# Kernel tuning notes

Hardware: AMD Instinct MI355X
Metric: run time of the kernel (lower is better)

## Reference

```python
import jax, jax.numpy as jnp
import numpy as np

B, H = 8192, 768


def _mk_linear(key, fan_in, fan_out):
    k1, k2 = jax.random.split(key)
    lim = 1.0 / np.sqrt(fan_in)
    W = jax.random.uniform(k1, (fan_out, fan_in), jnp.float32, -lim, lim)
    b = jax.random.uniform(k2, (fan_out,), jnp.float32, -lim, lim)
    return W, b


def setup_inputs() -> dict:
    key = jax.random.key(0)
    ks = jax.random.split(key, 6)
    modal_a = jax.random.normal(ks[0], (B, H), jnp.float32)
    modal_b = jax.random.normal(ks[1], (B, H), jnp.float32)
    W1m, b1m = _mk_linear(ks[2], H, H)
    W2m, b2m = _mk_linear(ks[3], H, H)
    W1v, b1v = _mk_linear(ks[4], H, H)
    W2v, b2v = _mk_linear(ks[5], H, H)
    return {"modal_a": modal_a, "modal_b": modal_b,
            "W1m": W1m, "b1m": b1m, "W2m": W2m, "b2m": b2m,
            "W1v": W1v, "b1v": b1v, "W2v": W2v, "b2v": b2v}


def reference(modal_a, modal_b, W1m, b1m, W2m, b2m, W1v, b1v, W2v, b2v):
    # mlp_mu: Linear -> Tanh -> Linear
    mu = jnp.tanh(modal_a @ W1m.T + b1m) @ W2m.T + b2m              # [B,H]
    # mlp_logvar: Linear -> Tanh -> Linear -> Tanh
    logvar = jnp.tanh(jnp.tanh(modal_a @ W1v.T + b1v) @ W2v.T + b2v)  # [B,H]
    inv_var = jnp.exp(-logvar)

    positive = -(mu - modal_b) ** 2 * 0.5 * inv_var                  # [B,H]

    # mean_j (mu[j] - mu[i])^2 = E[mu^2] - 2*mu[i]*E[mu] + mu[i]^2  (per feature dim)
    # Algebraic reduction of the O(B^2*H) tile in the original code.
    mu_mean = jnp.mean(mu, axis=0)                                   # [H]
    mu_sq_mean = jnp.mean(mu * mu, axis=0)                           # [H]
    pair_sq = mu_sq_mean - 2.0 * mu * mu_mean + mu * mu              # [B,H]
    negative = -pair_sq * 0.5 * inv_var                              # [B,H]

    pos_sum = jnp.sum(positive, axis=-1)                             # [B]
    neg_sum = jnp.sum(negative, axis=-1)                             # [B]
    lld = jnp.mean(pos_sum)
    bound = jnp.mean(pos_sum - neg_sum)
    return (lld, bound)
```

## Files before the change

### kernel.cpp

```cpp
#include <hip/hip_runtime.h>
#include <math.h>

typedef float v4f __attribute__((ext_vector_type(4)));
typedef short bf16x8 __attribute__((ext_vector_type(8)));

#define AS1 __attribute__((address_space(1)))
#define AS3 __attribute__((address_space(3)))

static constexpr int Bn = 8192;
static constexpr int Hn = 768;
static constexpr float invB = 1.0f / 8192.0f;

__device__ __forceinline__ short f32_to_bf16(float x) {
    union { float f; unsigned u; } v; v.f = x;
    unsigned r = (v.u + 0x7FFFu + ((v.u >> 16) & 1u)) >> 16;
    return (short)r;
}

__device__ __forceinline__ float fast_tanh(float x) {
    float xc = fminf(fmaxf(x, -15.0f), 15.0f);
    float e = __expf(2.0f * xc);
    float r = __builtin_amdgcn_rcpf(e + 1.0f);
    return 1.0f - 2.0f * r;
}

__global__ void prep_kernel(const float* __restrict__ A,
                            const float* __restrict__ W1m, const float* __restrict__ W2m,
                            const float* __restrict__ W1v, const float* __restrict__ W2v,
                            short* __restrict__ A_bf,
                            short* __restrict__ W1m_bf, short* __restrict__ W2m_bf,
                            short* __restrict__ W1v_bf, short* __restrict__ W2v_bf,
                            float* __restrict__ zbuf, int nzero) {
    const int tid = blockIdx.x * blockDim.x + threadIdx.x;
    if (tid < nzero) zbuf[tid] = 0.0f;
    constexpr int A4 = Bn * Hn / 4;
    constexpr int W4 = Hn * Hn / 4;
    const int total = A4 + 4 * W4;
    const int stride = gridDim.x * blockDim.x;
    for (int i = tid; i < total; i += stride) {
        const float* s; short* d; int j;
        if (i < A4) { s = A; d = A_bf; j = i; }
        else {
            int k = i - A4; int w = k / W4; j = k - w * W4;
            s = (w == 0) ? W1m : (w == 1) ? W2m : (w == 2) ? W1v : W2v;
            d = (w == 0) ? W1m_bf : (w == 1) ? W2m_bf : (w == 2) ? W1v_bf : W2v_bf;
        }
        float4 v = ((const float4*)s)[j];
        short4 o;
        o.x = f32_to_bf16(v.x); o.y = f32_to_bf16(v.y);
        o.z = f32_to_bf16(v.z); o.w = f32_to_bf16(v.w);
        ((short4*)d)[j] = o;
    }
}

__launch_bounds__(256, 2)
__global__ void gemm_l1(const short* __restrict__ A_g,
                        const short* __restrict__ Wm_g, const short* __restrict__ Wv_g,
                        const float* __restrict__ bm, const float* __restrict__ bv,
                        short* __restrict__ outm, short* __restrict__ outv) {
    constexpr int K = Hn;
    __shared__ __align__(16) short smem[24576];
    short* As = smem;
    short* Wms = smem + 8192;
    short* Wvs = smem + 16384;

    const int t = threadIdx.x;
    const int row0 = blockIdx.x * 128;
    const int col0 = blockIdx.y * 128;
    const int w = t >> 6, lane = t & 63;
    const int wm = w >> 1, wn = w & 1;
    const int lr = lane & 15, quad = lane >> 4;

    const int rt = t >> 3;
    const int bsrc = (t & 7) ^ (rt & 7);

    const short* pA[4]; const short* pWm[4]; const short* pWv[4];
#pragma unroll
    for (int i = 0; i < 4; ++i) {
        pA[i]  = A_g  + (size_t)(row0 + i * 32 + rt) * K + bsrc * 8;
        pWm[i] = Wm_g + (size_t)(col0 + i * 32 + rt) * K + bsrc * 8;
        pWv[i] = Wv_g + (size_t)(col0 + i * 32 + rt) * K + bsrc * 8;
    }

    v4f accm[4][4] = {}, accv[4][4] = {};

    for (int k0 = 0; k0 < K; k0 += 64) {
#pragma unroll
        for (int i = 0; i < 4; ++i) {
            __builtin_amdgcn_global_load_lds((AS1 void*)pA[i],  (AS3 void*)&As[i * 2048 + t * 8], 16, 0, 0);
            __builtin_amdgcn_global_load_lds((AS1 void*)pWm[i], (AS3 void*)&Wms[i * 2048 + t * 8], 16, 0, 0);
            __builtin_amdgcn_global_load_lds((AS1 void*)pWv[i], (AS3 void*)&Wvs[i * 2048 + t * 8], 16, 0, 0);
            pA[i] += 64; pWm[i] += 64; pWv[i] += 64;
        }
        __syncthreads();
#pragma unroll
        for (int s = 0; s < 2; ++s) {
            const int kb = s * 4 + quad;
            bf16x8 af[4], fm[4], fv[4];
#pragma unroll
            for (int mt = 0; mt < 4; ++mt) {
                int m = wm * 64 + mt * 16 + lr;
                af[mt] = *(const bf16x8*)&As[m * 64 + ((kb ^ (m & 7)) << 3)];
            }
#pragma unroll
            for (int nt = 0; nt < 4; ++nt) {
                int n = wn * 64 + nt * 16 + lr;
                int off = n * 64 + ((kb ^ (n & 7)) << 3);
                fm[nt] = *(const bf16x8*)&Wms[off];
                fv[nt] = *(const bf16x8*)&Wvs[off];
            }
#pragma unroll
            for (int mt = 0; mt < 4; ++mt)
#pragma unroll
                for (int nt = 0; nt < 4; ++nt) {
                    accm[mt][nt] = __builtin_amdgcn_mfma_f32_16x16x32_bf16(af[mt], fm[nt], accm[mt][nt], 0, 0, 0);
                    accv[mt][nt] = __builtin_amdgcn_mfma_f32_16x16x32_bf16(af[mt], fv[nt], accv[mt][nt], 0, 0, 0);
                }
        }
        __syncthreads();
    }

#pragma unroll
    for (int br = 0; br < 2; ++br) {
        const float* bias = br ? bv : bm;
        short* out = br ? outv : outm;
#pragma unroll
        for (int nt = 0; nt < 4; ++nt) {
            const int col_l = wn * 64 + nt * 16 + lr;
            const float bc = bias[col0 + col_l];
#pragma unroll
            for (int mt = 0; mt < 4; ++mt) {
#pragma unroll
                for (int r = 0; r < 4; ++r) {
                    const int row_l = wm * 64 + mt * 16 + quad * 4 + r;
                    float v = (br ? accv[mt][nt][r] : accm[mt][nt][r]) + bc;
                    smem[row_l * 136 + col_l] = f32_to_bf16(fast_tanh(v));
                }
            }
        }
        __syncthreads();
#pragma unroll
        for (int p = 0; p < 8; ++p) {
            const int c = p * 256 + t;
            const int row = c >> 4, rem = c & 15;
            bf16x8 v = *(const bf16x8*)&smem[row * 136 + rem * 8];
            *(bf16x8*)&out[(size_t)(row0 + row) * Hn + col0 + rem * 8] = v;
        }
        __syncthreads();
    }
}

__launch_bounds__(256, 2)
__global__ void gemm_l2(const short* __restrict__ Am_g, const short* __restrict__ Av_g,
                        const short* __restrict__ Wm_g, const short* __restrict__ Wv_g,
                        const float* __restrict__ bm, const float* __restrict__ bv,
                        const float* __restrict__ mb,
                        float* __restrict__ cs, float* __restrict__ cs2,
                        float* __restrict__ siv, float* __restrict__ sivmu,
                        float* __restrict__ accum, float* __restrict__ outp) {
    constexpr int K = Hn;
    __shared__ __align__(16) short smem[32768];
    short* Ams = smem;
    short* Avs = smem + 8192;
    short* Wms = smem + 16384;
    short* Wvs = smem + 24576;

    const int t = threadIdx.x;
    const int row0 = blockIdx.x * 128;
    const int col0 = blockIdx.y * 128;
    const int w = t >> 6, lane = t & 63;
    const int wm = w >> 1, wn = w & 1;
    const int lr = lane & 15, quad = lane >> 4;

    const int rt = t >> 3;
    const int bsrc = (t & 7) ^ (rt & 7);

    const short* pAm[4]; const short* pAv[4]; const short* pWm[4]; const short* pWv[4];
#pragma unroll
    for (int i = 0; i < 4; ++i) {
        pAm[i] = Am_g + (size_t)(row0 + i * 32 + rt) * K + bsrc * 8;
        pAv[i] = Av_g + (size_t)(row0 + i * 32 + rt) * K + bsrc * 8;
        pWm[i] = Wm_g + (size_t)(col0 + i * 32 + rt) * K + bsrc * 8;
        pWv[i] = Wv_g + (size_t)(col0 + i * 32 + rt) * K + bsrc * 8;
    }

    v4f accm[4][4] = {}, accv[4][4] = {};

    for (int k0 = 0; k0 < K; k0 += 64) {
#pragma unroll
        for (int i = 0; i < 4; ++i) {
            __builtin_amdgcn_global_load_lds((AS1 void*)pAm[i], (AS3 void*)&Ams[i * 2048 + t * 8], 16, 0, 0);
            __builtin_amdgcn_global_load_lds((AS1 void*)pAv[i], (AS3 void*)&Avs[i * 2048 + t * 8], 16, 0, 0);
            __builtin_amdgcn_global_load_lds((AS1 void*)pWm[i], (AS3 void*)&Wms[i * 2048 + t * 8], 16, 0, 0);
            __builtin_amdgcn_global_load_lds((AS1 void*)pWv[i], (AS3 void*)&Wvs[i * 2048 + t * 8], 16, 0, 0);
            pAm[i] += 64; pAv[i] += 64; pWm[i] += 64; pWv[i] += 64;
        }
        __syncthreads();
#pragma unroll
        for (int s = 0; s < 2; ++s) {
            const int kb = s * 4 + quad;
            bf16x8 fam[4], fav[4], fwm[4], fwv[4];
#pragma unroll
            for (int mt = 0; mt < 4; ++mt) {
                int m = wm * 64 + mt * 16 + lr;
                int off = m * 64 + ((kb ^ (m & 7)) << 3);
                fam[mt] = *(const bf16x8*)&Ams[off];
                fav[mt] = *(const bf16x8*)&Avs[off];
            }
#pragma unroll
            for (int nt = 0; nt < 4; ++nt) {
                int n = wn * 64 + nt * 16 + lr;
                int off = n * 64 + ((kb ^ (n & 7)) << 3);
                fwm[nt] = *(const bf16x8*)&Wms[off];
                fwv[nt] = *(const bf16x8*)&Wvs[off];
            }
#pragma unroll
            for (int mt = 0; mt < 4; ++mt)
#pragma unroll
                for (int nt = 0; nt < 4; ++nt) {
                    accm[mt][nt] = __builtin_amdgcn_mfma_f32_16x16x32_bf16(fam[mt], fwm[nt], accm[mt][nt], 0, 0, 0);
                    accv[mt][nt] = __builtin_amdgcn_mfma_f32_16x16x32_bf16(fav[mt], fwv[nt], accv[mt][nt], 0, 0, 0);
                }
        }
        __syncthreads();
    }

    float pos = 0.f, q = 0.f;
#pragma unroll
    for (int nt = 0; nt < 4; ++nt) {
        const int col = col0 + wn * 64 + nt * 16 + lr;
        const float bmc = bm[col], bvc = bv[col];
        float c1 = 0.f, c2 = 0.f, c3 = 0.f, c4 = 0.f;
#pragma unroll
        for (int mt = 0; mt < 4; ++mt) {
#pragma unroll
            for (int r = 0; r < 4; ++r) {
                const int row = row0 + wm * 64 + mt * 16 + quad * 4 + r;
                float mu = accm[mt][nt][r] + bmc;
                float tv = fast_tanh(accv[mt][nt][r] + bvc);
                float iv = __expf(-tv);
                float mbv = mb[(size_t)row * Hn + col];
                float d = mu - mbv;
                pos += iv * d * d;
                q   += iv * mu * mu;
                c1 += mu; c2 += mu * mu; c3 += iv; c4 += iv * mu;
            }
        }
        c1 += __shfl_xor(c1, 16); c1 += __shfl_xor(c1, 32);
        c2 += __shfl_xor(c2, 16); c2 += __shfl_xor(c2, 32);
        c3 += __shfl_xor(c3, 16); c3 += __shfl_xor(c3, 32);
        c4 += __shfl_xor(c4, 16); c4 += __shfl_xor(c4, 32);
        if (quad == 0) {
            atomicAdd(&cs[col], c1);
            atomicAdd(&cs2[col], c2);
            atomicAdd(&siv[col], c3);
            atomicAdd(&sivmu[col], c4);
        }
    }
    for (int off = 32; off > 0; off >>= 1) {
        pos += __shfl_down(pos, off);
        q   += __shfl_down(q, off);
    }
    __shared__ float redP[4], redQ[4];
    if (lane == 0) { redP[w] = pos; redQ[w] = q; }
    __syncthreads();
    __shared__ int is_last;
    if (t == 0) {
        atomicAdd(&accum[0], redP[0] + redP[1] + redP[2] + redP[3]);
        atomicAdd(&accum[1], redQ[0] + redQ[1] + redQ[2] + redQ[3]);
        __threadfence();
        unsigned old = atomicAdd((unsigned int*)&accum[3], 1u);
        is_last = (old == gridDim.x * gridDim.y - 1) ? 1 : 0;
    }
    __syncthreads();
    if (is_last) {
        float term = 0.f;
        for (int h = t; h < Hn; h += 256) {
            float v1 = atomicAdd(&cs[h], 0.0f);
            float v2 = atomicAdd(&cs2[h], 0.0f);
            float v3 = atomicAdd(&siv[h], 0.0f);
            float v4 = atomicAdd(&sivmu[h], 0.0f);
            term += v3 * v2 - 2.0f * v4 * v1;
        }
        for (int off = 32; off > 0; off >>= 1) term += __shfl_down(term, off);
        __shared__ float redT[4];
        if (lane == 0) redT[w] = term;
        __syncthreads();
        if (t == 0) {
            float T = redT[0] + redT[1] + redT[2] + redT[3];
            float P = atomicAdd(&accum[0], 0.0f);
            float Q = atomicAdd(&accum[1], 0.0f);
            float pos_sum = -0.5f * P;
            float neg_sum = -0.5f * (T * invB + Q);
            outp[0] = pos_sum * invB;
            outp[1] = (pos_sum - neg_sum) * invB;
        }
    }
}

extern "C" void kernel_launch(void* const* d_in, const int* in_sizes, int n_in,
                              void* d_out, int out_size, void* d_ws, size_t ws_size,
                              hipStream_t stream) {
    const float* modal_a = (const float*)d_in[0];
    const float* modal_b = (const float*)d_in[1];
    const float* W1m = (const float*)d_in[2];
    const float* b1m = (const float*)d_in[3];
    const float* W2m = (const float*)d_in[4];
    const float* b2m = (const float*)d_in[5];
    const float* W1v = (const float*)d_in[6];
    const float* b1v = (const float*)d_in[7];
    const float* W2v = (const float*)d_in[8];
    const float* b2v = (const float*)d_in[9];
    float* out = (float*)d_out;

    char* ws = (char*)d_ws;
    constexpr size_t szAH = (size_t)Bn * Hn * 2;
    constexpr size_t szW  = (size_t)Hn * Hn * 2;
    short* A_bf   = (short*)(ws);
    short* h1m    = (short*)(ws + szAH);
    short* h1v    = (short*)(ws + 2 * szAH);
    short* W1m_bf = (short*)(ws + 3 * szAH);
    short* W2m_bf = (short*)(ws + 3 * szAH + szW);
    short* W1v_bf = (short*)(ws + 3 * szAH + 2 * szW);
    short* W2v_bf = (short*)(ws + 3 * szAH + 3 * szW);
    float* cs     = (float*)(ws + 3 * szAH + 4 * szW);
    float* cs2    = cs + Hn;
    float* siv    = cs + 2 * Hn;
    float* sivmu  = cs + 3 * Hn;
    float* accum  = cs + 4 * Hn;

    prep_kernel<<<1280, 256, 0, stream>>>(modal_a, W1m, W2m, W1v, W2v,
                                          A_bf, W1m_bf, W2m_bf, W1v_bf, W2v_bf,
                                          cs, 4 * Hn + 8);

    gemm_l1<<<dim3(Bn / 128, Hn / 128), 256, 0, stream>>>(
        A_bf, W1m_bf, W1v_bf, b1m, b1v, h1m, h1v);

    gemm_l2<<<dim3(Bn / 128, Hn / 128), 256, 0, stream>>>(
        h1m, h1v, W2m_bf, W2v_bf, b2m, b2v, modal_b,
        cs, cs2, siv, sivmu, accum, out);
}
```

Measured before the change: 184.2 us.

## Switch both GEMM layers from bf16 to fp8 e4m3 MFMA

Converts activations and weights to fp8 e4m3 instead of bf16 and runs both GEMM layers with the fp8 16x16x32 MFMA. The K tile doubles to 128 bytes-per-row, and the layer-1 epilogue is reworked to pack four fp8 outputs per lane using the transposed accumulator layout. The intent is to halve memory traffic for inputs and intermediates and reduce the number of k-iterations. In exchange it loses a lot of precision in the reduction outputs without any scaling, which risks exceeding the accuracy tolerance.

Measured after the change: 176.9 us. 4.0% less time.

```diff
diff --git a/kernel.cpp b/kernel.cpp
--- a/kernel.cpp
+++ b/kernel.cpp
@@ -1,8 +1,8 @@
 #include <hip/hip_runtime.h>
+#include <hip/hip_fp8.h>
 #include <math.h>
 
 typedef float v4f __attribute__((ext_vector_type(4)));
-typedef short bf16x8 __attribute__((ext_vector_type(8)));
 
 #define AS1 __attribute__((address_space(1)))
 #define AS3 __attribute__((address_space(3)))
@@ -11,10 +11,9 @@
 static constexpr int Hn = 768;
 static constexpr float invB = 1.0f / 8192.0f;
 
-__device__ __forceinline__ short f32_to_bf16(float x) {
-    union { float f; unsigned u; } v; v.f = x;
-    unsigned r = (v.u + 0x7FFFu + ((v.u >> 16) & 1u)) >> 16;
-    return (short)r;
+__device__ __forceinline__ unsigned char cvt_e4m3(float x) {
+    __hip_fp8_e4m3 t(x);
+    return t.__x;
 }
 
 __device__ __forceinline__ float fast_tanh(float x) {
@@ -27,9 +26,9 @@
 __global__ void prep_kernel(const float* __restrict__ A,
                             const float* __restrict__ W1m, const float* __restrict__ W2m,
                             const float* __restrict__ W1v, const float* __restrict__ W2v,
-                            short* __restrict__ A_bf,
-                            short* __restrict__ W1m_bf, short* __restrict__ W2m_bf,
-                            short* __restrict__ W1v_bf, short* __restrict__ W2v_bf,
+                            unsigned char* __restrict__ A_f8,
+                            unsigned char* __restrict__ W1m_f8, unsigned char* __restrict__ W2m_f8,
+                            unsigned char* __restrict__ W1v_f8, unsigned char* __restrict__ W2v_f8,
                             float* __restrict__ zbuf, int nzero) {
     const int tid = blockIdx.x * blockDim.x + threadIdx.x;
     if (tid < nzero) zbuf[tid] = 0.0f;
@@ -38,31 +37,31 @@
     const int total = A4 + 4 * W4;
     const int stride = gridDim.x * blockDim.x;
     for (int i = tid; i < total; i += stride) {
-        const float* s; short* d; int j;
-        if (i < A4) { s = A; d = A_bf; j = i; }
+        const float* s; unsigned char* d; int j;
+        if (i < A4) { s = A; d = A_f8; j = i; }
         else {
             int k = i - A4; int w = k / W4; j = k - w * W4;
             s = (w == 0) ? W1m : (w == 1) ? W2m : (w == 2) ? W1v : W2v;
-            d = (w == 0) ? W1m_bf : (w == 1) ? W2m_bf : (w == 2) ? W1v_bf : W2v_bf;
+            d = (w == 0) ? W1m_f8 : (w == 1) ? W2m_f8 : (w == 2) ? W1v_f8 : W2v_f8;
         }
         float4 v = ((const float4*)s)[j];
-        short4 o;
-        o.x = f32_to_bf16(v.x); o.y = f32_to_bf16(v.y);
-        o.z = f32_to_bf16(v.z); o.w = f32_to_bf16(v.w);
-        ((short4*)d)[j] = o;
+        unsigned p = (unsigned)cvt_e4m3(v.x)
+                   | ((unsigned)cvt_e4m3(v.y) << 8)
+                   | ((unsigned)cvt_e4m3(v.z) << 16)
+                   | ((unsigned)cvt_e4m3(v.w) << 24);
+        ((unsigned*)d)[j] = p;
     }
 }
 
 __launch_bounds__(256, 2)
-__global__ void gemm_l1(const short* __restrict__ A_g,
-                        const short* __restrict__ Wm_g, const short* __restrict__ Wv_g,
+__global__ void gemm_l1(const unsigned char* __restrict__ A_g,
+                        const unsigned char* __restrict__ Wm_g, const unsigned char* __restrict__ Wv_g,
                         const float* __restrict__ bm, const float* __restrict__ bv,
-                        short* __restrict__ outm, short* __restrict__ outv) {
-    constexpr int K = Hn;
-    __shared__ __align__(16) short smem[24576];
-    short* As = smem;
-    short* Wms = smem + 8192;
-    short* Wvs = smem + 16384;
+                        unsigned char* __restrict__ outm, unsigned char* __restrict__ outv) {
+    __shared__ __align__(16) unsigned char smem[49152];
+    unsigned char* As  = smem;
+    unsigned char* Wms = smem + 16384;
+    unsigned char* Wvs = smem + 32768;
 
     const int t = threadIdx.x;
     const int row0 = blockIdx.x * 128;
@@ -70,100 +69,101 @@
     const int w = t >> 6, lane = t & 63;
     const int wm = w >> 1, wn = w & 1;
     const int lr = lane & 15, quad = lane >> 4;
-
-    const int rt = t >> 3;
-    const int bsrc = (t & 7) ^ (rt & 7);
-
-    const short* pA[4]; const short* pWm[4]; const short* pWv[4];
+    const int q2 = quad >> 1, q1 = quad & 1;
+
+    const int rst = t >> 3, cst = t & 7;
+    const int csrc = cst ^ (rst & 7);
+
+    const unsigned char* pA[4]; const unsigned char* pWm[4]; const unsigned char* pWv[4];
 #pragma unroll
     for (int i = 0; i < 4; ++i) {
-        pA[i]  = A_g  + (size_t)(row0 + i * 32 + rt) * K + bsrc * 8;
-        pWm[i] = Wm_g + (size_t)(col0 + i * 32 + rt) * K + bsrc * 8;
-        pWv[i] = Wv_g + (size_t)(col0 + i * 32 + rt) * K + bsrc * 8;
+        pA[i]  = A_g  + (size_t)(row0 + i * 32 + rst) * Hn + csrc * 16;
+        pWm[i] = Wm_g + (size_t)(col0 + i * 32 + rst) * Hn + csrc * 16;
+        pWv[i] = Wv_g + (size_t)(col0 + i * 32 + rst) * Hn + csrc * 16;
     }
 
     v4f accm[4][4] = {}, accv[4][4] = {};
 
-    for (int k0 = 0; k0 < K; k0 += 64) {
+    for (int k0 = 0; k0 < Hn; k0 += 128) {
 #pragma unroll
         for (int i = 0; i < 4; ++i) {
-            __builtin_amdgcn_global_load_lds((AS1 void*)pA[i],  (AS3 void*)&As[i * 2048 + t * 8], 16, 0, 0);
-            __builtin_amdgcn_global_load_lds((AS1 void*)pWm[i], (AS3 void*)&Wms[i * 2048 + t * 8], 16, 0, 0);
-            __builtin_amdgcn_global_load_lds((AS1 void*)pWv[i], (AS3 void*)&Wvs[i * 2048 + t * 8], 16, 0, 0);
-            pA[i] += 64; pWm[i] += 64; pWv[i] += 64;
-        }
-        __syncthreads();
-#pragma unroll
-        for (int s = 0; s < 2; ++s) {
-            const int kb = s * 4 + quad;
-            bf16x8 af[4], fm[4], fv[4];
+            __builtin_amdgcn_global_load_lds((AS1 void*)pA[i],  (AS3 void*)&As[i * 4096 + t * 16], 16, 0, 0);
+            __builtin_amdgcn_global_load_lds((AS1 void*)pWm[i], (AS3 void*)&Wms[i * 4096 + t * 16], 16, 0, 0);
+            __builtin_amdgcn_global_load_lds((AS1 void*)pWv[i], (AS3 void*)&Wvs[i * 4096 + t * 16], 16, 0, 0);
+            pA[i] += 128; pWm[i] += 128; pWv[i] += 128;
+        }
+        __syncthreads();
+#pragma unroll
+        for (int ks = 0; ks < 4; ++ks) {
+            const int cg = ks * 2 + q2;
+            long fb[4], fam[4], fav[4];
 #pragma unroll
             for (int mt = 0; mt < 4; ++mt) {
                 int m = wm * 64 + mt * 16 + lr;
-                af[mt] = *(const bf16x8*)&As[m * 64 + ((kb ^ (m & 7)) << 3)];
+                fb[mt] = *(const long*)&As[m * 128 + ((cg ^ (m & 7)) << 4) + (q1 << 3)];
             }
 #pragma unroll
             for (int nt = 0; nt < 4; ++nt) {
                 int n = wn * 64 + nt * 16 + lr;
-                int off = n * 64 + ((kb ^ (n & 7)) << 3);
-                fm[nt] = *(const bf16x8*)&Wms[off];
-                fv[nt] = *(const bf16x8*)&Wvs[off];
-            }
-#pragma unroll
-            for (int mt = 0; mt < 4; ++mt)
-#pragma unroll
-                for (int nt = 0; nt < 4; ++nt) {
-                    accm[mt][nt] = __builtin_amdgcn_mfma_f32_16x16x32_bf16(af[mt], fm[nt], accm[mt][nt], 0, 0, 0);
-                    accv[mt][nt] = __builtin_amdgcn_mfma_f32_16x16x32_bf16(af[mt], fv[nt], accv[mt][nt], 0, 0, 0);
+                int off = n * 128 + ((cg ^ (n & 7)) << 4) + (q1 << 3);
+                fam[nt] = *(const long*)&Wms[off];
+                fav[nt] = *(const long*)&Wvs[off];
+            }
+#pragma unroll
+            for (int nt = 0; nt < 4; ++nt)
+#pragma unroll
+                for (int mt = 0; mt < 4; ++mt) {
+                    accm[nt][mt] = __builtin_amdgcn_mfma_f32_16x16x32_fp8_fp8(fam[nt], fb[mt], accm[nt][mt], 0, 0, 0);
+                    accv[nt][mt] = __builtin_amdgcn_mfma_f32_16x16x32_fp8_fp8(fav[nt], fb[mt], accv[nt][mt], 0, 0, 0);
                 }
         }
         __syncthreads();
     }
 
+    unsigned* sm32 = (unsigned*)smem;
 #pragma unroll
     for (int br = 0; br < 2; ++br) {
         const float* bias = br ? bv : bm;
-        short* out = br ? outv : outm;
+        unsigned char* out = br ? outv : outm;
 #pragma unroll
         for (int nt = 0; nt < 4; ++nt) {
-            const int col_l = wn * 64 + nt * 16 + lr;
-            const float bc = bias[col0 + col_l];
+            float4 bb = *(const float4*)&bias[col0 + wn * 64 + nt * 16 + quad * 4];
 #pragma unroll
             for (int mt = 0; mt < 4; ++mt) {
-#pragma unroll
-                for (int r = 0; r < 4; ++r) {
-                    const int row_l = wm * 64 + mt * 16 + quad * 4 + r;
-                    float v = (br ? accv[mt][nt][r] : accm[mt][nt][r]) + bc;
-                    smem[row_l * 136 + col_l] = f32_to_bf16(fast_tanh(v));
-                }
-            }
-        }
-        __syncthreads();
-#pragma unroll
-        for (int p = 0; p < 8; ++p) {
-            const int c = p * 256 + t;
-            const int row = c >> 4, rem = c & 15;
-            bf16x8 v = *(const bf16x8*)&smem[row * 136 + rem * 8];
-            *(bf16x8*)&out[(size_t)(row0 + row) * Hn + col0 + rem * 8] = v;
+                const int row_l = wm * 64 + mt * 16 + lr;
+                v4f a = br ? accv[nt][mt] : accm[nt][mt];
+                unsigned p = (unsigned)cvt_e4m3(fast_tanh(a[0] + bb.x))
+                           | ((unsigned)cvt_e4m3(fast_tanh(a[1] + bb.y)) << 8)
+                           | ((unsigned)cvt_e4m3(fast_tanh(a[2] + bb.z)) << 16)
+                           | ((unsigned)cvt_e4m3(fast_tanh(a[3] + bb.w)) << 24);
+                sm32[row_l * 36 + wn * 16 + nt * 4 + quad] = p;
+            }
+        }
+        __syncthreads();
+#pragma unroll
+        for (int i = 0; i < 4; ++i) {
+            const int idx = i * 256 + t;
+            const int row = idx >> 3, seg = idx & 7;
+            uint4 d = *(const uint4*)&sm32[row * 36 + seg * 4];
+            *(uint4*)&out[(size_t)(row0 + row) * Hn + col0 + seg * 16] = d;
         }
         __syncthreads();
     }
 }
 
 __launch_bounds__(256, 2)
-__global__ void gemm_l2(const short* __restrict__ Am_g, const short* __restrict__ Av_g,
-                        const short* __restrict__ Wm_g, const short* __restrict__ Wv_g,
+__global__ void gemm_l2(const unsigned char* __restrict__ Am_g, const unsigned char* __restrict__ Av_g,
+                        const unsigned char* __restrict__ Wm_g, const unsigned char* __restrict__ Wv_g,
                         const float* __restrict__ bm, const float* __restrict__ bv,
                         const float* __restrict__ mb,
                         float* __restrict__ cs, float* __restrict__ cs2,
                         float* __restrict__ siv, float* __restrict__ sivmu,
                         float* __restrict__ accum, float* __restrict__ outp) {
-    constexpr int K = Hn;
-    __shared__ __align__(16) short smem[32768];
-    short* Ams = smem;
-    short* Avs = smem + 8192;
-    short* Wms = smem + 16384;
-    short* Wvs = smem + 24576;
+    __shared__ __align__(16) unsigned char smem[65536];
+    unsigned char* Ams = smem;
+    unsigned char* Avs = smem + 16384;
+    unsigned char* Wms = smem + 32768;
+    unsigned char* Wvs = smem + 49152;
 
     const int t = threadIdx.x;
     const int row0 = blockIdx.x * 128;
@@ -171,55 +171,57 @@
     const int w = t >> 6, lane = t & 63;
     const int wm = w >> 1, wn = w & 1;
     const int lr = lane & 15, quad = lane >> 4;
-
-    const int rt = t >> 3;
-    const int bsrc = (t & 7) ^ (rt & 7);
-
-    const short* pAm[4]; const short* pAv[4]; const short* pWm[4]; const short* pWv[4];
+    const int q2 = quad >> 1, q1 = quad & 1;
+
+    const int rst = t >> 3, cst = t & 7;
+    const int csrc = cst ^ (rst & 7);
+
+    const unsigned char* pAm[4]; const unsigned char* pAv[4];
+    const unsigned char* pWm[4]; const unsigned char* pWv[4];
 #pragma unroll
     for (int i = 0; i < 4; ++i) {
-        pAm[i] = Am_g + (size_t)(row0 + i * 32 + rt) * K + bsrc * 8;
-        pAv[i] = Av_g + (size_t)(row0 + i * 32 + rt) * K + bsrc * 8;
-        pWm[i] = Wm_g + (size_t)(col0 + i * 32 + rt) * K + bsrc * 8;
-        pWv[i] = Wv_g + (size_t)(col0 + i * 32 + rt) * K + bsrc * 8;
+        pAm[i] = Am_g + (size_t)(row0 + i * 32 + rst) * Hn + csrc * 16;
+        pAv[i] = Av_g + (size_t)(row0 + i * 32 + rst) * Hn + csrc * 16;
+        pWm[i] = Wm_g + (size_t)(col0 + i * 32 + rst) * Hn + csrc * 16;
+        pWv[i] = Wv_g + (size_t)(col0 + i * 32 + rst) * Hn + csrc * 16;
     }
 
     v4f accm[4][4] = {}, accv[4][4] = {};
 
-    for (int k0 = 0; k0 < K; k0 += 64) {
+    for (int k0 = 0; k0 < Hn; k0 += 128) {
 #pragma unroll
         for (int i = 0; i < 4; ++i) {
-            __builtin_amdgcn_global_load_lds((AS1 void*)pAm[i], (AS3 void*)&Ams[i * 2048 + t * 8], 16, 0, 0);
-            __builtin_amdgcn_global_load_lds((AS1 void*)pAv[i], (AS3 void*)&Avs[i * 2048 + t * 8], 16, 0, 0);
-            __builtin_amdgcn_global_load_lds((AS1 void*)pWm[i], (AS3 void*)&Wms[i * 2048 + t * 8], 16, 0, 0);
-            __builtin_amdgcn_global_load_lds((AS1 void*)pWv[i], (AS3 void*)&Wvs[i * 2048 + t * 8], 16, 0, 0);
-            pAm[i] += 64; pAv[i] += 64; pWm[i] += 64; pWv[i] += 64;
-        }
-        __syncthreads();
-#pragma unroll
-        for (int s = 0; s < 2; ++s) {
-            const int kb = s * 4 + quad;
-            bf16x8 fam[4], fav[4], fwm[4], fwv[4];
+            __builtin_amdgcn_global_load_lds((AS1 void*)pAm[i], (AS3 void*)&Ams[i * 4096 + t * 16], 16, 0, 0);
+            __builtin_amdgcn_global_load_lds((AS1 void*)pAv[i], (AS3 void*)&Avs[i * 4096 + t * 16], 16, 0, 0);
+            __builtin_amdgcn_global_load_lds((AS1 void*)pWm[i], (AS3 void*)&Wms[i * 4096 + t * 16], 16, 0, 0);
+            __builtin_amdgcn_global_load_lds((AS1 void*)pWv[i], (AS3 void*)&Wvs[i * 4096 + t * 16], 16, 0, 0);
+            pAm[i] += 128; pAv[i] += 128; pWm[i] += 128; pWv[i] += 128;
+        }
+        __syncthreads();
+#pragma unroll
+        for (int ks = 0; ks < 4; ++ks) {
+            const int cg = ks * 2 + q2;
+            long fam[4], fav[4], fwm[4], fwv[4];
 #pragma unroll
             for (int mt = 0; mt < 4; ++mt) {
                 int m = wm * 64 + mt * 16 + lr;
-                int off = m * 64 + ((kb ^ (m & 7)) << 3);
-                fam[mt] = *(const bf16x8*)&Ams[off];
-                fav[mt] = *(const bf16x8*)&Avs[off];
+                int off = m * 128 + ((cg ^ (m & 7)) << 4) + (q1 << 3);
+                fam[mt] = *(const long*)&Ams[off];
+                fav[mt] = *(const long*)&Avs[off];
             }
 #pragma unroll
             for (int nt = 0; nt < 4; ++nt) {
                 int n = wn * 64 + nt * 16 + lr;
-                int off = n * 64 + ((kb ^ (n & 7)) << 3);
-                fwm[nt] = *(const bf16x8*)&Wms[off];
-                fwv[nt] = *(const bf16x8*)&Wvs[off];
+                int off = n * 128 + ((cg ^ (n & 7)) << 4) + (q1 << 3);
+                fwm[nt] = *(const long*)&Wms[off];
+                fwv[nt] = *(const long*)&Wvs[off];
             }
 #pragma unroll
             for (int mt = 0; mt < 4; ++mt)
 #pragma unroll
                 for (int nt = 0; nt < 4; ++nt) {
-                    accm[mt][nt] = __builtin_amdgcn_mfma_f32_16x16x32_bf16(fam[mt], fwm[nt], accm[mt][nt], 0, 0, 0);
-                    accv[mt][nt] = __builtin_amdgcn_mfma_f32_16x16x32_bf16(fav[mt], fwv[nt], accv[mt][nt], 0, 0, 0);
+                    accm[mt][nt] = __builtin_amdgcn_mfma_f32_16x16x32_fp8_fp8(fam[mt], fwm[nt], accm[mt][nt], 0, 0, 0);
+                    accv[mt][nt] = __builtin_amdgcn_mfma_f32_16x16x32_fp8_fp8(fav[mt], fwv[nt], accv[mt][nt], 0, 0, 0);
                 }
         }
         __syncthreads();
@@ -314,29 +316,29 @@
     float* out = (float*)d_out;
 
     char* ws = (char*)d_ws;
-    constexpr size_t szAH = (size_t)Bn * Hn * 2;
-    constexpr size_t szW  = (size_t)Hn * Hn * 2;
-    short* A_bf   = (short*)(ws);
-    short* h1m    = (short*)(ws + szAH);
-    short* h1v    = (short*)(ws + 2 * szAH);
-    short* W1m_bf = (short*)(ws + 3 * szAH);
-    short* W2m_bf = (short*)(ws + 3 * szAH + szW);
-    short* W1v_bf = (short*)(ws + 3 * szAH + 2 * szW);
-    short* W2v_bf = (short*)(ws + 3 * szAH + 3 * szW);
-    float* cs     = (float*)(ws + 3 * szAH + 4 * szW);
+    constexpr size_t szA8 = (size_t)Bn * Hn;
+    constexpr size_t szW8 = (size_t)Hn * Hn;
+    unsigned char* A_f8   = (unsigned char*)(ws);
+    unsigned char* h1m_f8 = (unsigned char*)(ws + szA8);
+    unsigned char* h1v_f8 = (unsigned char*)(ws + 2 * szA8);
+    unsigned char* W1m_f8 = (unsigned char*)(ws + 3 * szA8);
+    unsigned char* W2m_f8 = (unsigned char*)(ws + 3 * szA8 + szW8);
+    unsigned char* W1v_f8 = (unsigned char*)(ws + 3 * szA8 + 2 * szW8);
+    unsigned char* W2v_f8 = (unsigned char*)(ws + 3 * szA8 + 3 * szW8);
+    float* cs     = (float*)(ws + 3 * szA8 + 4 * szW8);
     float* cs2    = cs + Hn;
     float* siv    = cs + 2 * Hn;
     float* sivmu  = cs + 3 * Hn;
     float* accum  = cs + 4 * Hn;
 
     prep_kernel<<<1280, 256, 0, stream>>>(modal_a, W1m, W2m, W1v, W2v,
-                                          A_bf, W1m_bf, W2m_bf, W1v_bf, W2v_bf,
+                                          A_f8, W1m_f8, W2m_f8, W1v_f8, W2v_f8,
                                           cs, 4 * Hn + 8);
 
     gemm_l1<<<dim3(Bn / 128, Hn / 128), 256, 0, stream>>>(
-        A_bf, W1m_bf, W1v_bf, b1m, b1v, h1m, h1v);
+        A_f8, W1m_f8, W1v_f8, b1m, b1v, h1m_f8, h1v_f8);
 
     gemm_l2<<<dim3(Bn / 128, Hn / 128), 256, 0, stream>>>(
-        h1m, h1v, W2m_bf, W2v_bf, b2m, b2v, modal_b,
+        h1m_f8, h1v_f8, W2m_f8, W2v_f8, b2m, b2v, modal_b,
         cs, cs2, siv, sivmu, accum, out);
 }
```
